# Optimization experiments

Measured on AMD Instinct MI355X. Metric: run time of the kernel, lower is better.

## Reference

```python
import jax, jax.numpy as jnp
import numpy as np

DIM = 1024
NUM_HEADS = 16
HEAD_DIM = DIM // NUM_HEADS  # 64


def setup_inputs() -> dict:
    key = jax.random.key(0)
    k1, k2, k3 = jax.random.split(key, 3)
    B, N, C = 4, 2048, DIM
    x = jax.random.normal(k1, (B, N, C), dtype=jnp.float32)
    W_qkv = jax.random.normal(k2, (C, 3 * C), dtype=jnp.float32) * (1.0 / np.sqrt(C))
    b_qkv = jnp.zeros((3 * C,), dtype=jnp.float32)
    W_proj = jax.random.normal(k3, (C, C), dtype=jnp.float32) * (1.0 / np.sqrt(C))
    b_proj = jnp.zeros((C,), dtype=jnp.float32)
    return {"x": x, "W_qkv": W_qkv, "b_qkv": b_qkv, "W_proj": W_proj, "b_proj": b_proj}


def reference(x, W_qkv, b_qkv, W_proj, b_proj):
    B, N, C = x.shape
    H, D = NUM_HEADS, HEAD_DIM
    # QKV projection: [B,N,3C] -> [3,B,H,N,D]
    qkv = x @ W_qkv + b_qkv
    qkv = qkv.reshape(B, N, 3, H, D).transpose(2, 0, 3, 1, 4)
    q, k, v = qkv[0], qkv[1], qkv[2]
    scale = 1.0 / jnp.sqrt(jnp.asarray(D, dtype=x.dtype))
    # scores: [B,H,N,N]
    attn = jnp.einsum("bhqd,bhkd->bhqk", q, k) * scale
    attn = jax.nn.softmax(attn, axis=-1)
    # weighted sum: [B,H,N,D] -> [B,N,C]
    out = jnp.einsum("bhqk,bhkd->bhqd", attn, v)
    out = out.transpose(0, 2, 1, 3).reshape(B, N, C)
    return out @ W_proj + b_proj
```

## Files before the change

### kernel.cpp

```cpp
#include <hip/hip_runtime.h>
#include <stdint.h>

typedef _Float16 f16;
typedef _Float16 f16x8 __attribute__((ext_vector_type(8)));
typedef _Float16 f16x4 __attribute__((ext_vector_type(4)));
typedef __fp16 h2 __attribute__((ext_vector_type(2)));
typedef float floatx4 __attribute__((ext_vector_type(4)));
typedef int intx4 __attribute__((ext_vector_type(4)));

#define MFMA16(A, B, C) __builtin_amdgcn_mfma_f32_16x16x32_f16(A, B, C, 0, 0, 0)

#if __has_builtin(__builtin_amdgcn_exp2f)
#define EXP2(x) __builtin_amdgcn_exp2f(x)
#else
#define EXP2(x) exp2f(x)
#endif

__device__ __forceinline__ void g2l16(const void* gptr, void* lptr) {
  const unsigned loff = __builtin_amdgcn_readfirstlane((unsigned)(unsigned long long)lptr);
  __builtin_amdgcn_global_load_lds(
      (const __attribute__((address_space(1))) unsigned int*)gptr,
      (__attribute__((address_space(3))) unsigned int*)loff,
      16, 0, 0);
}


__global__ __launch_bounds__(256) void cast_x(const float* __restrict__ x,
                                              f16* __restrict__ xo) {
  const int idx = blockIdx.x * 256 + threadIdx.x;
  const float4* p = (const float4*)x + (size_t)idx * 2;
  const float4 a = p[0], b = p[1];
  f16x8 o;
  o[0] = (f16)a.x; o[1] = (f16)a.y; o[2] = (f16)a.z; o[3] = (f16)a.w;
  o[4] = (f16)b.x; o[5] = (f16)b.y; o[6] = (f16)b.z; o[7] = (f16)b.w;
  *((f16x8*)xo + idx) = o;
}

__global__ __launch_bounds__(256) void transpose_cast(const float* __restrict__ W,
                                                      f16* __restrict__ Wt, int cols) {
  __shared__ f16 tile[64][72];
  const int t = threadIdx.x;
  const int nt = blockIdx.x, kt = blockIdx.y;
  const int c4 = (t & 15) * 4;
#pragma unroll
  for (int it = 0; it < 4; ++it) {
    const int r = it * 16 + (t >> 4);
    const float4 v = *(const float4*)(W + (size_t)(kt * 64 + r) * cols + nt * 64 + c4);
    tile[r][c4 + 0] = (f16)v.x;
    tile[r][c4 + 1] = (f16)v.y;
    tile[r][c4 + 2] = (f16)v.z;
    tile[r][c4 + 3] = (f16)v.w;
  }
  __syncthreads();
#pragma unroll
  for (int it = 0; it < 4; ++it) {
    const int n = it * 16 + (t >> 4);
    f16x4 o;
#pragma unroll
    for (int e = 0; e < 4; ++e) o[e] = tile[c4 + e][n];
    *(f16x4*)(Wt + (size_t)(nt * 64 + n) * 1024 + kt * 64 + c4) = o;
  }
}

__device__ __forceinline__ void swizzle_mn(int bid, int& mi, int& ni) {
  const int xcd = bid & 7;
  const int slot = bid >> 3;
  mi = xcd * 8 + (slot & 7);
  ni = slot >> 3;
}


__device__ __forceinline__ void gemm_core(const f16* __restrict__ A,
                                          const f16* __restrict__ Bt,
                                          int m0, int n0, char* smem,
                                          floatx4 (&acc)[4][4]) {
  const int tid = threadIdx.x;
  const int lane = tid & 63;
  const int wave = tid >> 6;
  const int wr = (wave >> 1) * 64;
  const int wc = (wave & 1) * 64;
  const int rsub = lane >> 3;
  const int csub = lane & 7;

  const f16* gp[8];
  int lofs[8];
#pragma unroll
  for (int ci = 0; ci < 8; ++ci) {
    const int ch = wave * 8 + ci;
    const int within = ch & 15;
    const int r = within * 8 + rsub;
    const int gc = csub ^ (r & 7);
    gp[ci] = (ch < 16 ? (A + (size_t)(m0 + r) * 1024)
                      : (Bt + (size_t)(n0 + r) * 1024)) + gc * 8;
    lofs[ci] = ch * 1024;
  }

  const int fr = lane & 15;
  const int fq = lane >> 4;

#pragma unroll
  for (int ci = 0; ci < 8; ++ci) g2l16(gp[ci], smem + lofs[ci]);

#pragma unroll 1
  for (int kt = 0; kt < 16; ++kt) {
    __builtin_amdgcn_s_waitcnt(0);
    __syncthreads();
    if (kt < 15) {
      char* nbuf = smem + ((kt + 1) & 1) * 32768;
#pragma unroll
      for (int ci = 0; ci < 8; ++ci)
        g2l16(gp[ci] + (size_t)(kt + 1) * 64, nbuf + lofs[ci]);
    }
    const char* buf = smem + (kt & 1) * 32768;

#pragma unroll
    for (int ks = 0; ks < 2; ++ks) {
      f16x8 av[4], bv[4];
#pragma unroll
      for (int i = 0; i < 4; ++i) {
        const int ra = wr + i * 16 + fr;
        const int ca = (ks * 4 + fq) ^ (ra & 7);
        av[i] = *(const f16x8*)(buf + ra * 128 + ca * 16);
        const int rb = wc + i * 16 + fr;
        const int cb = (ks * 4 + fq) ^ (rb & 7);
        bv[i] = *(const f16x8*)(buf + 16384 + rb * 128 + cb * 16);
      }
#pragma unroll
      for (int i = 0; i < 4; ++i)
#pragma unroll
        for (int j = 0; j < 4; ++j)
          acc[i][j] = MFMA16(av[i], bv[j], acc[i][j]);
    }
  }
}

#define QSCALE 0.18033688011112042f

__global__ __launch_bounds__(256) void gemm_qkv(const f16* __restrict__ A,
                                                const f16* __restrict__ Bt,
                                                const float* __restrict__ bias,
                                                f16* __restrict__ qb,
                                                f16* __restrict__ kb,
                                                f16* __restrict__ vtb) {
  __shared__ __align__(16) char smem[65536];
  floatx4 acc[4][4];
#pragma unroll
  for (int i = 0; i < 4; ++i)
#pragma unroll
    for (int j = 0; j < 4; ++j)
#pragma unroll
      for (int r = 0; r < 4; ++r) acc[i][j][r] = 0.f;

  int mi, ni;
  swizzle_mn(blockIdx.x, mi, ni);
  const int m0 = mi * 128, n0 = ni * 128;
  gemm_core(A, Bt, m0, n0, smem, acc);

  const int lane = threadIdx.x & 63, wave = threadIdx.x >> 6;
  const int wr = (wave >> 1) * 64, wc = (wave & 1) * 64;
  const int fr = lane & 15, fq = lane >> 4;
  const int sec = n0 >> 10;
#pragma unroll
  for (int i = 0; i < 4; ++i) {
    const int mb = m0 + wr + i * 16 + fq * 4;
    const int b = mb >> 11;
    const int s = mb & 2047;
#pragma unroll
    for (int j = 0; j < 4; ++j) {
      const int n = n0 + wc + j * 16 + fr;
      const float bs = bias[n];
      const int nn = n & 1023;
      const int h = nn >> 6, d = nn & 63;
      const int bh = b * 16 + h;
      if (sec == 0) {
#pragma unroll
        for (int r = 0; r < 4; ++r)
          qb[((size_t)bh * 2048 + s + r) * 64 + d] = (f16)((acc[i][j][r] + bs) * QSCALE);
      } else if (sec == 1) {
#pragma unroll
        for (int r = 0; r < 4; ++r)
          kb[((size_t)bh * 2048 + s + r) * 64 + d] = (f16)(acc[i][j][r] + bs);
      } else {
        f16x4 pk;
#pragma unroll
        for (int r = 0; r < 4; ++r) pk[r] = (f16)(acc[i][j][r] + bs);
        *(f16x4*)(vtb + ((size_t)bh * 64 + d) * 2048 + s) = pk;
      }
    }
  }
}

__global__ __launch_bounds__(256) void gemm_proj(const f16* __restrict__ A,
                                                 const f16* __restrict__ Bt,
                                                 const float* __restrict__ bias,
                                                 float* __restrict__ out) {
  __shared__ __align__(16) char smem[65536];
  floatx4 acc[4][4];
#pragma unroll
  for (int i = 0; i < 4; ++i)
#pragma unroll
    for (int j = 0; j < 4; ++j)
#pragma unroll
      for (int r = 0; r < 4; ++r) acc[i][j][r] = 0.f;

  int mi, ni;
  swizzle_mn(blockIdx.x, mi, ni);
  const int m0 = mi * 128, n0 = ni * 128;
  gemm_core(A, Bt, m0, n0, smem, acc);

  const int lane = threadIdx.x & 63, wave = threadIdx.x >> 6;
  const int wr = (wave >> 1) * 64, wc = (wave & 1) * 64;
  const int fr = lane & 15, fq = lane >> 4;
#pragma unroll
  for (int i = 0; i < 4; ++i) {
    const int mb = m0 + wr + i * 16 + fq * 4;
#pragma unroll
    for (int j = 0; j < 4; ++j) {
      const int n = n0 + wc + j * 16 + fr;
      const float bs = bias[n];
#pragma unroll
      for (int r = 0; r < 4; ++r)
        out[(size_t)(mb + r) * 1024 + n] = acc[i][j][r] + bs;
    }
  }
}


__global__ __launch_bounds__(256, 2) void attn_kernel(const f16* __restrict__ qb,
                                                      const f16* __restrict__ kg,
                                                      const f16* __restrict__ vtb,
                                                      f16* __restrict__ ob) {
  __shared__ __align__(16) char smem[65536];
  const int tid = threadIdx.x, lane = tid & 63, wave = tid >> 6;
  const int fr = lane & 15, fq = lane >> 4;
  const int bid = blockIdx.x;
  const int xcd = bid & 7;
  const int slot = bid >> 3;
  const int qt = slot & 15;
  const int bh = (slot >> 4) * 8 + xcd;
  const f16* Q = qb + (size_t)bh * 2048 * 64;
  const f16* K = kg + (size_t)bh * 2048 * 64;
  const f16* Vt = vtb + (size_t)bh * 64 * 2048;
  const int q0 = qt * 128 + wave * 32;

  f16x8 bq[2][2];
#pragma unroll
  for (int ic = 0; ic < 2; ++ic)
#pragma unroll
    for (int ks = 0; ks < 2; ++ks)
      bq[ic][ks] = *(const f16x8*)(Q + (size_t)(q0 + ic * 16 + fr) * 64 + ks * 32 + fq * 8);

  const bool isK = wave < 2;
  const f16* gp[8];
  int lofs[8];
#pragma unroll
  for (int ci = 0; ci < 8; ++ci) {
    const int ch = wave * 8 + ci;
    if (isK) {
      const int r = ch * 8 + (lane >> 3);
      const int gc = (lane & 7) ^ (r & 7);
      gp[ci] = K + (size_t)r * 64 + gc * 8;
      lofs[ci] = ch * 1024;
    } else {
      const int cv = ch - 16;
      const int dd = cv * 4 + (lane >> 4);
      const int gc = (lane & 15) ^ (dd & 15);
      gp[ci] = Vt + (size_t)dd * 2048 + gc * 8;
      lofs[ci] = 16384 + cv * 1024;
    }
  }
  const size_t kstep = isK ? 8192 : 128;

  floatx4 oacc[2][4];
  float psum[2] = {0.f, 0.f};
  const floatx4 fzero = {0.f, 0.f, 0.f, 0.f};
  const h2 hones = {(__fp16)1.0f, (__fp16)1.0f};
#pragma unroll
  for (int ic = 0; ic < 2; ++ic)
#pragma unroll
    for (int dt = 0; dt < 4; ++dt)
#pragma unroll
      for (int r = 0; r < 4; ++r) oacc[ic][dt][r] = 0.f;

#pragma unroll
  for (int ci = 0; ci < 8; ++ci) g2l16(gp[ci], smem + lofs[ci]);

#pragma unroll 1
  for (int kt = 0; kt < 16; ++kt) {
    __builtin_amdgcn_s_waitcnt(0);
    __syncthreads();
    if (kt < 15) {
      char* nbuf = smem + ((kt + 1) & 1) * 32768;
#pragma unroll
      for (int ci = 0; ci < 8; ++ci)
        g2l16(gp[ci] + (size_t)(kt + 1) * kstep, nbuf + lofs[ci]);
    }
    const char* kl = smem + (kt & 1) * 32768;
    const char* vl = kl + 16384;

    floatx4 sacc[2][8];
    {
      f16x8 ak[8];
#pragma unroll
      for (int jr = 0; jr < 8; ++jr) {
        const int row = jr * 16 + fr;
        const int cc = fq ^ (row & 7);
        ak[jr] = *(const f16x8*)(kl + row * 128 + cc * 16);
      }
#pragma unroll
      for (int ic = 0; ic < 2; ++ic)
#pragma unroll
        for (int jr = 0; jr < 8; ++jr)
          sacc[ic][jr] = MFMA16(ak[jr], bq[ic][0], fzero);
    }
    {
      f16x8 ak[8];
#pragma unroll
      for (int jr = 0; jr < 8; ++jr) {
        const int row = jr * 16 + fr;
        const int cc = (4 + fq) ^ (row & 7);
        ak[jr] = *(const f16x8*)(kl + row * 128 + cc * 16);
      }
#pragma unroll
      for (int ic = 0; ic < 2; ++ic)
#pragma unroll
        for (int jr = 0; jr < 8; ++jr)
          sacc[ic][jr] = MFMA16(ak[jr], bq[ic][1], sacc[ic][jr]);
    }

    int pkx[2][8], pky[2][8];
#pragma unroll
    for (int ic = 0; ic < 2; ++ic)
#pragma unroll
      for (int jr = 0; jr < 8; ++jr) {
        floatx4 e;
#pragma unroll
        for (int r = 0; r < 4; ++r) e[r] = EXP2(sacc[ic][jr][r]);
        const auto lo = __builtin_amdgcn_cvt_pkrtz(e[0], e[1]);
        const auto hi = __builtin_amdgcn_cvt_pkrtz(e[2], e[3]);
        pkx[ic][jr] = __builtin_bit_cast(int, lo);
        pky[ic][jr] = __builtin_bit_cast(int, hi);
#if __has_builtin(__builtin_amdgcn_fdot2)
        psum[ic] = __builtin_amdgcn_fdot2(__builtin_bit_cast(h2, pkx[ic][jr]), hones,
                                          psum[ic], false);
        psum[ic] = __builtin_amdgcn_fdot2(__builtin_bit_cast(h2, pky[ic][jr]), hones,
                                          psum[ic], false);
#else
        psum[ic] += (e[0] + e[1]) + (e[2] + e[3]);
#endif
      }

#pragma unroll
    for (int kb = 0; kb < 4; ++kb) {
      f16x8 av[4];
      const int c0 = 4 * kb + (fq >> 1);
      const int c1 = c0 + 2;
      const int off0 = (fq & 1) * 8;
      const int off1 = off0 ^ 8;
#pragma unroll
      for (int dt = 0; dt < 4; ++dt) {
        const int row = dt * 16 + fr;
        const char* rb = vl + row * 256;
        const f16x4 lo = *(const f16x4*)(rb + ((c0 ^ fr) * 16 + off0));
        const f16x4 hi = *(const f16x4*)(rb + ((c1 ^ fr) * 16 + off1));
        f16x8 v;
        v[0] = lo[0]; v[1] = lo[1]; v[2] = lo[2]; v[3] = lo[3];
        v[4] = hi[0]; v[5] = hi[1]; v[6] = hi[2]; v[7] = hi[3];
        av[dt] = v;
      }
#pragma unroll
      for (int ic = 0; ic < 2; ++ic) {
        intx4 t;
        t[0] = pkx[ic][2 * kb];
        t[1] = pky[ic][2 * kb];
        t[2] = __shfl_xor(pkx[ic][2 * kb + 1], 16, 64);
        t[3] = __shfl_xor(pky[ic][2 * kb + 1], 16, 64);
        const f16x8 bp = __builtin_bit_cast(f16x8, t);
#pragma unroll
        for (int dt = 0; dt < 4; ++dt)
          oacc[ic][dt] = MFMA16(av[dt], bp, oacc[ic][dt]);
      }
    }
  }

  float inv[2];
#pragma unroll
  for (int ic = 0; ic < 2; ++ic) {
    float s = psum[ic];
    s += __shfl_xor(s, 16, 64);
    s += __shfl_xor(s, 32, 64);
    inv[ic] = 1.0f / s;
  }

  char* pb = smem + wave * 4096;
#pragma unroll
  for (int ic = 0; ic < 2; ++ic)
#pragma unroll
    for (int dt = 0; dt < 4; ++dt) {
      f16x4 w;
#pragma unroll
      for (int r = 0; r < 4; ++r) w[r] = (f16)(oacc[ic][dt][r] * inv[ic]);
      const int row = ic * 16 + fr;
      const int dgrp = dt * 2 + (fq >> 1);
      const int chunk = dgrp ^ (fr & 7);
      *(f16x4*)(pb + row * 128 + chunk * 16 + (fq & 1) * 8) = w;
    }
  __syncthreads();
  const int b = bh >> 4, hh = bh & 15;
#pragma unroll
  for (int it = 0; it < 4; ++it) {
    const int rq = it * 8 + (lane >> 3);
    const int c8 = lane & 7;
    const f16x8 v = *(const f16x8*)(pb + rq * 128 + (c8 ^ (rq & 7)) * 16);
    *(f16x8*)(ob + ((size_t)b * 2048 + q0 + rq) * 1024 + hh * 64 + c8 * 8) = v;
  }
}


extern "C" void kernel_launch(void* const* d_in, const int* in_sizes, int n_in,
                              void* d_out, int out_size, void* d_ws, size_t ws_size,
                              hipStream_t stream) {
  (void)in_sizes; (void)n_in; (void)out_size; (void)ws_size;
  const float* x = (const float*)d_in[0];
  const float* Wqkv = (const float*)d_in[1];
  const float* bqkv = (const float*)d_in[2];
  const float* Wproj = (const float*)d_in[3];
  const float* bproj = (const float*)d_in[4];
  float* out = (float*)d_out;

  char* ws = (char*)d_ws;
  f16* xb    = (f16*)(ws);
  f16* wqkvt = (f16*)(ws + ((size_t)16 << 20));
  f16* wprjt = (f16*)(ws + ((size_t)22 << 20));
  f16* qb    = (f16*)(ws + ((size_t)24 << 20));
  f16* kb    = (f16*)(ws + ((size_t)40 << 20));
  f16* vtb   = (f16*)(ws + ((size_t)56 << 20));
  f16* ob    = (f16*)(ws + ((size_t)72 << 20));

  cast_x<<<4096, 256, 0, stream>>>(x, xb);
  transpose_cast<<<dim3(48, 16), 256, 0, stream>>>(Wqkv, wqkvt, 3072);
  transpose_cast<<<dim3(16, 16), 256, 0, stream>>>(Wproj, wprjt, 1024);
  gemm_qkv<<<1536, 256, 0, stream>>>(xb, wqkvt, bqkv, qb, kb, vtb);
  attn_kernel<<<1024, 256, 0, stream>>>(qb, kb, vtb, ob);
  gemm_proj<<<512, 256, 0, stream>>>(ob, wprjt, bproj, out);
}
```

Before: 288.6 us.

## Single-buffer GEMM LDS, stage Q/K epilogue through LDS, and use permlane16_swap for P

The GEMM core drops its double-buffered LDS prefetch in favour of a single 32KB buffer: each k-step loads, waits and syncs before computing. This halves LDS use, which may raise occupancy, but global-load latency is no longer overlapped with MFMA work. The QKV epilogue for Q and K now writes each tile into swizzled LDS and then emits coalesced 16-byte stores per head row, replacing scattered 2-byte stores. In attention, V fragments are read with one 16-byte LDS load instead of two 8-byte loads, and the P operand is rearranged with permlane16_swap in place of shuffles, which changes the k-index pairing to match.

```diff
diff --git a/kernel.cpp b/kernel.cpp
--- a/kernel.cpp
+++ b/kernel.cpp
@@ -7,6 +7,7 @@
 typedef __fp16 h2 __attribute__((ext_vector_type(2)));
 typedef float floatx4 __attribute__((ext_vector_type(4)));
 typedef int intx4 __attribute__((ext_vector_type(4)));
+typedef unsigned int uint2v __attribute__((ext_vector_type(2)));
 
 #define MFMA16(A, B, C) __builtin_amdgcn_mfma_f32_16x16x32_f16(A, B, C, 0, 0, 0)
 
@@ -83,7 +84,7 @@
   const int csub = lane & 7;
 
   const f16* gp[8];
-  int lofs[8];
+  char* lp[8];
 #pragma unroll
   for (int ci = 0; ci < 8; ++ci) {
     const int ch = wave * 8 + ci;
@@ -92,26 +93,19 @@
     const int gc = csub ^ (r & 7);
     gp[ci] = (ch < 16 ? (A + (size_t)(m0 + r) * 1024)
                       : (Bt + (size_t)(n0 + r) * 1024)) + gc * 8;
-    lofs[ci] = ch * 1024;
+    lp[ci] = smem + ch * 1024;
   }
 
   const int fr = lane & 15;
   const int fq = lane >> 4;
 
-#pragma unroll
-  for (int ci = 0; ci < 8; ++ci) g2l16(gp[ci], smem + lofs[ci]);
-
 #pragma unroll 1
   for (int kt = 0; kt < 16; ++kt) {
+    __syncthreads();
+#pragma unroll
+    for (int ci = 0; ci < 8; ++ci) g2l16(gp[ci] + kt * 64, lp[ci]);
     __builtin_amdgcn_s_waitcnt(0);
     __syncthreads();
-    if (kt < 15) {
-      char* nbuf = smem + ((kt + 1) & 1) * 32768;
-#pragma unroll
-      for (int ci = 0; ci < 8; ++ci)
-        g2l16(gp[ci] + (size_t)(kt + 1) * 64, nbuf + lofs[ci]);
-    }
-    const char* buf = smem + (kt & 1) * 32768;
 
 #pragma unroll
     for (int ks = 0; ks < 2; ++ks) {
@@ -120,10 +114,10 @@
       for (int i = 0; i < 4; ++i) {
         const int ra = wr + i * 16 + fr;
         const int ca = (ks * 4 + fq) ^ (ra & 7);
-        av[i] = *(const f16x8*)(buf + ra * 128 + ca * 16);
+        av[i] = *(const f16x8*)(smem + ra * 128 + ca * 16);
         const int rb = wc + i * 16 + fr;
         const int cb = (ks * 4 + fq) ^ (rb & 7);
-        bv[i] = *(const f16x8*)(buf + 16384 + rb * 128 + cb * 16);
+        bv[i] = *(const f16x8*)(smem + 16384 + rb * 128 + cb * 16);
       }
 #pragma unroll
       for (int i = 0; i < 4; ++i)
@@ -142,7 +136,7 @@
                                                 f16* __restrict__ qb,
                                                 f16* __restrict__ kb,
                                                 f16* __restrict__ vtb) {
-  __shared__ __align__(16) char smem[65536];
+  __shared__ __align__(16) char smem[32768];
   floatx4 acc[4][4];
 #pragma unroll
   for (int i = 0; i < 4; ++i)
@@ -156,35 +150,61 @@
   const int m0 = mi * 128, n0 = ni * 128;
   gemm_core(A, Bt, m0, n0, smem, acc);
 
-  const int lane = threadIdx.x & 63, wave = threadIdx.x >> 6;
+  const int tid = threadIdx.x;
+  const int lane = tid & 63, wave = tid >> 6;
   const int wr = (wave >> 1) * 64, wc = (wave & 1) * 64;
   const int fr = lane & 15, fq = lane >> 4;
   const int sec = n0 >> 10;
-#pragma unroll
-  for (int i = 0; i < 4; ++i) {
-    const int mb = m0 + wr + i * 16 + fq * 4;
-    const int b = mb >> 11;
-    const int s = mb & 2047;
-#pragma unroll
-    for (int j = 0; j < 4; ++j) {
-      const int n = n0 + wc + j * 16 + fr;
-      const float bs = bias[n];
-      const int nn = n & 1023;
-      const int h = nn >> 6, d = nn & 63;
-      const int bh = b * 16 + h;
-      if (sec == 0) {
-#pragma unroll
-        for (int r = 0; r < 4; ++r)
-          qb[((size_t)bh * 2048 + s + r) * 64 + d] = (f16)((acc[i][j][r] + bs) * QSCALE);
-      } else if (sec == 1) {
-#pragma unroll
-        for (int r = 0; r < 4; ++r)
-          kb[((size_t)bh * 2048 + s + r) * 64 + d] = (f16)(acc[i][j][r] + bs);
-      } else {
+
+  if (sec < 2) {
+    f16* dst = (sec == 0) ? qb : kb;
+    const float scale = (sec == 0) ? QSCALE : 1.0f;
+    __syncthreads();
+#pragma unroll
+    for (int i = 0; i < 4; ++i) {
+      const int mbs = wr + i * 16 + fq * 4;
+#pragma unroll
+      for (int j = 0; j < 4; ++j) {
+        const int n_l = wc + j * 16 + fr;
+        const float bs = bias[n0 + n_l];
+#pragma unroll
+        for (int r = 0; r < 4; ++r) {
+          const int m_l = mbs + r;
+          const int chunkW = (n_l >> 3) ^ (m_l & 7);
+          *(f16*)(smem + m_l * 256 + chunkW * 16 + (n_l & 7) * 2) =
+              (f16)((acc[i][j][r] + bs) * scale);
+        }
+      }
+    }
+    __syncthreads();
+    const int h0 = (n0 & 1023) >> 6;
+#pragma unroll
+    for (int t = 0; t < 8; ++t) {
+      const int hh = t >> 2, mg = t & 3;
+      const int m_l = mg * 32 + (tid >> 3);
+      const int cR = hh * 8 + (tid & 7);
+      const int cL = cR ^ (m_l & 7);
+      const f16x8 v = *(const f16x8*)(smem + m_l * 256 + cL * 16);
+      const int mb = m0 + m_l;
+      const int b = mb >> 11, s = mb & 2047;
+      *(f16x8*)(dst + (((size_t)(b * 16 + h0 + hh) * 2048 + s) * 64) + (tid & 7) * 8) = v;
+    }
+  } else {
+#pragma unroll
+    for (int i = 0; i < 4; ++i) {
+      const int mb = m0 + wr + i * 16 + fq * 4;
+      const int b = mb >> 11;
+      const int s = mb & 2047;
+#pragma unroll
+      for (int j = 0; j < 4; ++j) {
+        const int n = n0 + wc + j * 16 + fr;
+        const float bs = bias[n];
+        const int nn = n & 1023;
+        const int h = nn >> 6, d = nn & 63;
         f16x4 pk;
 #pragma unroll
         for (int r = 0; r < 4; ++r) pk[r] = (f16)(acc[i][j][r] + bs);
-        *(f16x4*)(vtb + ((size_t)bh * 64 + d) * 2048 + s) = pk;
+        *(f16x4*)(vtb + ((size_t)(b * 16 + h) * 64 + d) * 2048 + s) = pk;
       }
     }
   }
@@ -194,7 +214,7 @@
                                                  const f16* __restrict__ Bt,
                                                  const float* __restrict__ bias,
                                                  float* __restrict__ out) {
-  __shared__ __align__(16) char smem[65536];
+  __shared__ __align__(16) char smem[32768];
   floatx4 acc[4][4];
 #pragma unroll
   for (int i = 0; i < 4; ++i)
@@ -282,6 +302,8 @@
 #pragma unroll
       for (int r = 0; r < 4; ++r) oacc[ic][dt][r] = 0.f;
 
+  const int pg = ((fq & 1) << 1) | (fq >> 1);
+
 #pragma unroll
   for (int ci = 0; ci < 8; ++ci) g2l16(gp[ci], smem + lofs[ci]);
 
@@ -353,28 +375,31 @@
 #pragma unroll
     for (int kb = 0; kb < 4; ++kb) {
       f16x8 av[4];
-      const int c0 = 4 * kb + (fq >> 1);
-      const int c1 = c0 + 2;
-      const int off0 = (fq & 1) * 8;
-      const int off1 = off0 ^ 8;
 #pragma unroll
       for (int dt = 0; dt < 4; ++dt) {
         const int row = dt * 16 + fr;
-        const char* rb = vl + row * 256;
-        const f16x4 lo = *(const f16x4*)(rb + ((c0 ^ fr) * 16 + off0));
-        const f16x4 hi = *(const f16x4*)(rb + ((c1 ^ fr) * 16 + off1));
-        f16x8 v;
-        v[0] = lo[0]; v[1] = lo[1]; v[2] = lo[2]; v[3] = lo[3];
-        v[4] = hi[0]; v[5] = hi[1]; v[6] = hi[2]; v[7] = hi[3];
-        av[dt] = v;
+        av[dt] = *(const f16x8*)(vl + row * 256 + (((4 * kb + pg) ^ fr) * 16));
       }
 #pragma unroll
       for (int ic = 0; ic < 2; ++ic) {
         intx4 t;
-        t[0] = pkx[ic][2 * kb];
-        t[1] = pky[ic][2 * kb];
-        t[2] = __shfl_xor(pkx[ic][2 * kb + 1], 16, 64);
-        t[3] = __shfl_xor(pky[ic][2 * kb + 1], 16, 64);
+#if __has_builtin(__builtin_amdgcn_permlane16_swap)
+        const uint2v sx = __builtin_amdgcn_permlane16_swap(
+            (unsigned)pkx[ic][2 * kb], (unsigned)pkx[ic][2 * kb + 1], false, false);
+        const uint2v sy = __builtin_amdgcn_permlane16_swap(
+            (unsigned)pky[ic][2 * kb], (unsigned)pky[ic][2 * kb + 1], false, false);
+        t[0] = (int)sx[0]; t[1] = (int)sy[0]; t[2] = (int)sx[1]; t[3] = (int)sy[1];
+#else
+        const int xs = __shfl_xor(pkx[ic][2 * kb], 16, 64);
+        const int ys = __shfl_xor(pkx[ic][2 * kb + 1], 16, 64);
+        const int xs2 = __shfl_xor(pky[ic][2 * kb], 16, 64);
+        const int ys2 = __shfl_xor(pky[ic][2 * kb + 1], 16, 64);
+        const bool odd = (fq & 1) != 0;
+        t[0] = odd ? ys : pkx[ic][2 * kb];
+        t[1] = odd ? ys2 : pky[ic][2 * kb];
+        t[2] = odd ? pkx[ic][2 * kb + 1] : xs;
+        t[3] = odd ? pky[ic][2 * kb + 1] : xs2;
+#endif
         const f16x8 bp = __builtin_bit_cast(f16x8, t);
 #pragma unroll
         for (int dt = 0; dt < 4; ++dt)
```

Result: faster. 264.3 us (-8.4%).
